# Performance work log

Measured on AMD Instinct MI355X. Metric: run time of the kernel, lower is better.

The kernel has to match this reference:

```python
import jax, jax.numpy as jnp
import numpy as np

B, L, H, A, C = 16, 2048, 1024, 1024, 5  # batch, seq_len, hidden, attention_size, num_cat_choices


def setup_inputs() -> dict:
    key = jax.random.key(0)
    ks = jax.random.split(key, 5)
    inp = jax.random.normal(ks[0], (B, L, H), dtype=jnp.float32)
    W_hidden = jax.random.normal(ks[1], (A, H), dtype=jnp.float32) * 0.02
    b_hidden = jnp.zeros((A,), jnp.float32)
    query = jax.random.normal(ks[2], (A, 1), dtype=jnp.float32) * 0.02
    W_cls = jax.random.normal(ks[3], (1, H), dtype=jnp.float32) * 0.02
    b_cls = jnp.zeros((1,), jnp.float32)
    # Build masks with exactly C marker positions per row (required by the
    # original nested-loop logic: C markers -> C segments, count in [0, C-1]).
    rng = np.random.default_rng(0)
    attn = np.zeros((B, L), np.int64)
    mlm = np.zeros((B, L), np.int64)
    for b in range(B):
        end = max(int(L - rng.integers(0, L // 4)), 64)  # valid length
        attn[b, :end] = 1
        seg = (end - 4) // C
        for c in range(C):
            mlm[b, 2 + c * seg] = 1
    return dict(input=inp, attention_mask=jnp.asarray(attn),
                mlm_mask=jnp.asarray(mlm), W_hidden=W_hidden,
                b_hidden=b_hidden, query=query, W_cls=W_cls, b_cls=b_cls)


def reference(input, attention_mask, mlm_mask, W_hidden, b_hidden, query, W_cls, b_cls):
    # --- attention merge (dropout is identity at eval) ---
    keys = jnp.tanh(input @ W_hidden.T + b_hidden)                    # (B,L,A)
    qvar = jnp.var(query, ddof=1)                                     # torch.var default: unbiased
    probs = (keys @ query) / jnp.sqrt(A * qvar)                       # (B,L,1)
    mask = (1.0 - attention_mask[..., None].astype(jnp.float32)) * -1000.0
    att = jax.nn.softmax(probs * mask, axis=1)                        # faithful: logits are probs*mask
    vals = att + input                                                # (B,L,H)
    # --- vectorized replacement of the nested segment-mask loop (roberta branch) ---
    idx = jnp.arange(L)
    marker = jnp.where(mlm_mask > 0, idx, L)                          # (B,L)
    starts = jnp.sort(marker, axis=1)[:, :C]                          # (B,C) marker positions
    end_idx = attention_mask.sum(axis=1)                              # (B,)
    # segment c covers [starts[c]+1, next_boundary); boundary = next marker - 1,
    # last segment's boundary = end_idx - 1  (mlm_mask_extend[i,c,start+1:j-1]=1)
    bounds = jnp.concatenate([starts[:, 1:] - 1, (end_idx - 1)[:, None]], axis=1)  # (B,C)
    seg_mask = ((idx[None, None, :] >= starts[:, :, None] + 1)
                & (idx[None, None, :] < bounds[:, :, None])).astype(vals.dtype)    # (B,C,L)
    # fused segment pooling: avoids materializing the (B,C,L,H) repeat
    context = jnp.einsum('bcl,blh->bch', seg_mask, vals)              # (B,C,H)
    logits = context @ W_cls.T + b_cls                                # (B,C,1)
    return logits
```

## Files before the change

### kernel.cpp

```cpp
#include <hip/hip_runtime.h>
#include <hip/hip_bf16.h>
#include <math.h>

#define B_ 16
#define L_ 2048
#define H_ 1024
#define A_ 1024
#define C_ 5

#define NSPLIT 4
#define MT 32
#define KPH 256
#define TPB 16
#define KC_BLOCKS (B_ * TPB * NSPLIT)
#define KE_BLOCKS (B_ * L_ / 16)
#define KW_BLOCKS 256
#define PBS 8
#define PROBE_THRESH 150.0f

typedef __attribute__((ext_vector_type(8))) short short8v;
typedef __attribute__((ext_vector_type(4))) float float4v;

static constexpr size_t OFF_SCAL   = 0;
static constexpr size_t OFF_END    = 64;
static constexpr size_t OFF_CNT    = 192;
static constexpr size_t OFF_STARTS = 320;
static constexpr size_t OFF_LIST   = 4096;
static constexpr size_t OFF_WF     = OFF_LIST + (size_t)B_ * L_ * 4;
static constexpr size_t OFF_PP     = OFF_WF + (size_t)A_ * H_ * 2;
static constexpr size_t OFF_D      = OFF_PP + (size_t)NSPLIT * B_ * L_ * 4;
static constexpr size_t OFF_PROBE  = OFF_D + (size_t)B_ * L_ * 4;

static __device__ __forceinline__ unsigned short f2bf(float f) {
  unsigned u = __float_as_uint(f);
  unsigned r = (u >> 16) & 1u;
  return (unsigned short)((u + 0x7fffu + r) >> 16);
}

__global__ __launch_bounds__(256) void kWA(const int* __restrict__ attn,
                                           const int* __restrict__ mlm,
                                           const float* __restrict__ query,
                                           const float* __restrict__ Wcls,
                                           const float* __restrict__ Wh,
                                           const float* __restrict__ inp,
                                           float* __restrict__ ws_scal,
                                           int* __restrict__ endv,
                                           int* __restrict__ cnt,
                                           int* __restrict__ starts,
                                           int* __restrict__ list,
                                           unsigned short* __restrict__ Wfrag,
                                           float* __restrict__ d) {
  __shared__ int   wsh[4];
  __shared__ float sf1[256];
  __shared__ float sf2[256];
  const int bid = blockIdx.x;
  const int t = threadIdx.x;
  const int w = t >> 6;
  const int lane = t & 63;

  if (bid < KE_BLOCKS) {
    const int r0 = bid * 16 + w * 4;
    const int a0v = attn[r0], a1v = attn[r0 + 1], a2v = attn[r0 + 2], a3v = attn[r0 + 3];
    if ((a0v | a1v | a2v | a3v) == 0) return;
    float4 wv4[4];
#pragma unroll
    for (int k = 0; k < 4; ++k) wv4[k] = *(const float4*)(Wcls + k * 256 + lane * 4);
    const float* p0 = inp + (size_t)r0 * H_;
    float4 x0[4], x1[4], x2[4], x3[4];
    if (a0v) {
#pragma unroll
      for (int k = 0; k < 4; ++k) x0[k] = *(const float4*)(p0 + k * 256 + lane * 4);
    }
    if (a1v) {
#pragma unroll
      for (int k = 0; k < 4; ++k) x1[k] = *(const float4*)(p0 + H_ + k * 256 + lane * 4);
    }
    if (a2v) {
#pragma unroll
      for (int k = 0; k < 4; ++k) x2[k] = *(const float4*)(p0 + 2 * H_ + k * 256 + lane * 4);
    }
    if (a3v) {
#pragma unroll
      for (int k = 0; k < 4; ++k) x3[k] = *(const float4*)(p0 + 3 * H_ + k * 256 + lane * 4);
    }
#define DOTROW(XV, AV, IDX)                                                          \
    if (AV) {                                                                        \
      float acc = 0.f;                                                               \
      _Pragma("unroll")                                                              \
      for (int k = 0; k < 4; ++k)                                                    \
        acc += XV[k].x * wv4[k].x + XV[k].y * wv4[k].y +                             \
               XV[k].z * wv4[k].z + XV[k].w * wv4[k].w;                              \
      _Pragma("unroll")                                                              \
      for (int o = 1; o < 64; o <<= 1) acc += __shfl_xor(acc, o, 64);                \
      if (lane == 0) d[r0 + IDX] = acc;                                              \
    }
    DOTROW(x0, a0v, 0)
    DOTROW(x1, a1v, 1)
    DOTROW(x2, a2v, 2)
    DOTROW(x3, a3v, 3)
#undef DOTROW
    return;
  }

  const int g = bid - KE_BLOCKS;
  if (g < B_) {
    const int b = g;
    const int* arow = attn + (size_t)b * L_;
    const int* mrow = mlm + (size_t)b * L_;
    const int base = t * 8;

    int loc[8];
    int lc = 0;
#pragma unroll
    for (int j = 0; j < 8; ++j) {
      int l = base + j;
      if (arow[l] == 0) loc[lc++] = l;
    }
    int incl = lc;
#pragma unroll
    for (int o = 1; o < 64; o <<= 1) {
      int v = __shfl_up(incl, o, 64);
      if (lane >= o) incl += v;
    }
    if (lane == 63) wsh[w] = incl;
    __syncthreads();
    int pre = 0, total = 0;
#pragma unroll
    for (int i = 0; i < 4; ++i) {
      int s = wsh[i];
      if (i < w) pre += s;
      total += s;
    }
    int excl = pre + incl - lc;
    int* lrow = list + (size_t)b * L_;
    for (int j = 0; j < lc; ++j) lrow[excl + j] = loc[j];
    if (t == 0) {
      cnt[b] = total;
      endv[b] = L_ - total;
    }
    __syncthreads();

    int mloc[8];
    int mc = 0;
#pragma unroll
    for (int j = 0; j < 8; ++j) {
      int l = base + j;
      if (mrow[l] > 0) mloc[mc++] = l;
    }
    int incl2 = mc;
#pragma unroll
    for (int o = 1; o < 64; o <<= 1) {
      int v = __shfl_up(incl2, o, 64);
      if (lane >= o) incl2 += v;
    }
    if (lane == 63) wsh[w] = incl2;
    __syncthreads();
    int pre2 = 0;
#pragma unroll
    for (int i = 0; i < 4; ++i) {
      if (i < w) pre2 += wsh[i];
    }
    int excl2 = pre2 + incl2 - mc;
    for (int j = 0; j < mc; ++j) {
      int idx = excl2 + j;
      if (idx < C_) starts[b * C_ + idx] = mloc[j];
    }
  } else if (g == B_) {
    float s = 0.f, s2 = 0.f;
    for (int i = t; i < A_; i += 256) {
      float q = query[i];
      s += q;
      s2 = fmaf(q, q, s2);
    }
    sf1[t] = s;
    sf2[t] = s2;
    __syncthreads();
    for (int off = 128; off >= 1; off >>= 1) {
      if (t < off) {
        sf1[t] += sf1[t + off];
        sf2[t] += sf2[t + off];
      }
      __syncthreads();
    }
    float qsum = sf1[0], qsq = sf2[0];
    __syncthreads();
    float wv = 0.f;
    for (int i = t; i < H_; i += 256) wv += Wcls[i];
    sf1[t] = wv;
    __syncthreads();
    for (int off = 128; off >= 1; off >>= 1) {
      if (t < off) sf1[t] += sf1[t + off];
      __syncthreads();
    }
    if (t == 0) {
      float var = (qsq - qsum * qsum / (float)A_) / (float)(A_ - 1);
      ws_scal[0] = sqrtf((float)A_ * var);
      ws_scal[1] = sf1[0];
    }
  } else {
    const int g4 = g - B_ - 1;
    const int ga = g4 >> 2;
    const int q = g4 & 3;
    const int row = ga * 16 + (lane & 15);
    const int colb = (lane >> 4) * 8;
    const float* srcrow = Wh + (size_t)row * H_;
#pragma unroll
    for (int i = 0; i < 2; ++i) {
      const int kb = q * 8 + w * 2 + i;
      const float* src = srcrow + kb * 32 + colb;
      float4 u0 = *(const float4*)src;
      float4 u1 = *(const float4*)(src + 4);
      union { short8v v; unsigned short h[8]; } o;
      o.h[0] = f2bf(u0.x); o.h[1] = f2bf(u0.y); o.h[2] = f2bf(u0.z); o.h[3] = f2bf(u0.w);
      o.h[4] = f2bf(u1.x); o.h[5] = f2bf(u1.y); o.h[6] = f2bf(u1.z); o.h[7] = f2bf(u1.w);
      *(short8v*)(Wfrag + (((size_t)ga * 32 + kb) * 64 + lane) * 8) = o.v;
    }
  }
}

__global__ __launch_bounds__(256) void kProbe(const float* __restrict__ inp,
                                              const unsigned short* __restrict__ Wfrag,
                                              const float* __restrict__ bh,
                                              const float* __restrict__ query,
                                              const int* __restrict__ cnt,
                                              const int* __restrict__ list,
                                              float* __restrict__ probe) {
  __shared__ __align__(16) unsigned short Xs[16][KPH + 8];
  __shared__ float red[4][16];
  const int bid = blockIdx.x;
  const int b = bid >> 3;
  const int sl = bid & 7;
  const int t = threadIdx.x;
  const int c0 = cnt[b];
  const int w = t >> 6;
  const int lane = t & 63;
  const int lg = lane >> 4;
  const int lc = lane & 15;

  const int srow = t >> 4;
  const int scol = (t & 15) * 16;
  int pi = srow;
  if (pi >= c0) pi = (c0 > 0) ? (c0 - 1) : 0;
  const int xl = (c0 > 0) ? list[(size_t)b * L_ + pi] : 0;
  const float* xptr = inp + ((size_t)(b * L_ + xl)) * H_ + scol;

  const unsigned short* wf = Wfrag + ((size_t)(sl * 8 + w * 2) * 32) * 512 + lane * 8;

  float4v acc0 = (float4v){0.f, 0.f, 0.f, 0.f};
  float4v acc1 = (float4v){0.f, 0.f, 0.f, 0.f};

  for (int ph = 0; ph < H_ / KPH; ++ph) {
    __syncthreads();
#pragma unroll
    for (int j = 0; j < 2; ++j) {
      float4 u0 = *(const float4*)(xptr + ph * KPH + j * 8);
      float4 u1 = *(const float4*)(xptr + ph * KPH + j * 8 + 4);
      union { short8v v; unsigned short h[8]; } o;
      o.h[0] = f2bf(u0.x); o.h[1] = f2bf(u0.y); o.h[2] = f2bf(u0.z); o.h[3] = f2bf(u0.w);
      o.h[4] = f2bf(u1.x); o.h[5] = f2bf(u1.y); o.h[6] = f2bf(u1.z); o.h[7] = f2bf(u1.w);
      *(short8v*)&Xs[srow][scol + j * 8] = o.v;
    }
    __syncthreads();
#pragma unroll
    for (int kk = 0; kk < 8; ++kk) {
      const int kb = ph * 8 + kk;
      short8v bv0 = *(const short8v*)(wf + (size_t)kb * 512);
      short8v bv1 = *(const short8v*)(wf + (size_t)kb * 512 + 32 * 512);
      short8v av = *(const short8v*)&Xs[lc][kk * 32 + lg * 8];
      acc0 = __builtin_amdgcn_mfma_f32_16x16x32_bf16(av, bv0, acc0, 0, 0, 0);
      acc1 = __builtin_amdgcn_mfma_f32_16x16x32_bf16(av, bv1, acc1, 0, 0, 0);
    }
  }

  float pp[4] = {0.f, 0.f, 0.f, 0.f};
  {
    const int ag0 = sl * 128 + w * 32 + lc;
    const float q0 = query[ag0];
    const float b0 = bh[ag0];
    const int ag1 = ag0 + 16;
    const float q1 = query[ag1];
    const float b1 = bh[ag1];
#pragma unroll
    for (int r = 0; r < 4; ++r) {
      pp[r] = fmaf(tanhf(acc0[r] + b0), q0, pp[r]);
      pp[r] = fmaf(tanhf(acc1[r] + b1), q1, pp[r]);
    }
  }
#pragma unroll
  for (int r = 0; r < 4; ++r) {
#pragma unroll
    for (int o = 1; o < 16; o <<= 1)
      pp[r] += __shfl_xor(pp[r], o, 64);
  }
  __syncthreads();
  if (lc == 0) {
#pragma unroll
    for (int r = 0; r < 4; ++r) red[w][lg * 4 + r] = pp[r];
  }
  __syncthreads();
  if (t < 16) {
    float s = red[0][t] + red[1][t] + red[2][t] + red[3][t];
    probe[((size_t)b * PBS + sl) * 16 + t] = (c0 > 0) ? s : 0.f;
  }
}

__global__ __launch_bounds__(256, 4) void kMain(const float* __restrict__ inp,
                                                const unsigned short* __restrict__ Wfrag,
                                                const float* __restrict__ bh,
                                                const float* __restrict__ query,
                                                const int* __restrict__ cnt,
                                                const int* __restrict__ list,
                                                const float* __restrict__ ws_scal,
                                                const float* __restrict__ probe,
                                                float* __restrict__ probpart) {
  __shared__ __align__(16) unsigned short Xs[MT][KPH + 8];
  __shared__ float red[4][MT];
  __shared__ int sskip;

  const int bid = blockIdx.x;
  const int t = threadIdx.x;
  const int w = t >> 6;
  const int lane = t & 63;

  const int as = (bid >> 3) & 3;
  const int T = (bid & 7) | ((bid >> 5) << 3);
  const int b = T >> 4;
  const int tile = T & 15;
  const int c0 = cnt[b];
  if (tile * MT >= c0) return;

  if (t == 0) sskip = 0;
  __syncthreads();
  if (t < 16) {
    float s = 0.f;
#pragma unroll
    for (int p8 = 0; p8 < PBS; ++p8) s += probe[((size_t)b * PBS + p8) * 16 + t];
    float logit = -1000.0f * (s / ws_scal[0]);
    if (logit >= PROBE_THRESH) atomicOr(&sskip, 1);
  }
  __syncthreads();
  if (sskip) return;

  const int lg = lane >> 4;
  const int lc = lane & 15;

  const int srow = t >> 3;
  const int scol = (t & 7) * 32;
  const int gi = tile * MT + srow;
  const int gidx = (gi < c0) ? gi : (c0 - 1);
  const int xl = list[(size_t)b * L_ + gidx];
  const float* xptr = inp + ((size_t)(b * L_ + xl)) * H_ + scol;

  const unsigned short* wfbase = Wfrag + ((size_t)(as * 16 + w * 4) * 32) * 512 + lane * 8;

  float4v acc[2][4];
#pragma unroll
  for (int m = 0; m < 2; ++m)
#pragma unroll
    for (int n = 0; n < 4; ++n) acc[m][n] = (float4v){0.f, 0.f, 0.f, 0.f};

  for (int ph = 0; ph < H_ / KPH; ++ph) {
    __syncthreads();
#pragma unroll
    for (int j = 0; j < 4; ++j) {
      float4 u0 = *(const float4*)(xptr + ph * KPH + j * 8);
      float4 u1 = *(const float4*)(xptr + ph * KPH + j * 8 + 4);
      union { short8v v; unsigned short h[8]; } o;
      o.h[0] = f2bf(u0.x); o.h[1] = f2bf(u0.y); o.h[2] = f2bf(u0.z); o.h[3] = f2bf(u0.w);
      o.h[4] = f2bf(u1.x); o.h[5] = f2bf(u1.y); o.h[6] = f2bf(u1.z); o.h[7] = f2bf(u1.w);
      *(short8v*)&Xs[srow][scol + j * 8] = o.v;
    }
    __syncthreads();

    const unsigned short* fp0 = wfbase + (size_t)(ph * 8) * 512;
    short8v cb0 = *(const short8v*)(fp0);
    short8v cb1 = *(const short8v*)(fp0 + 32 * 512);
    short8v cb2 = *(const short8v*)(fp0 + 64 * 512);
    short8v cb3 = *(const short8v*)(fp0 + 96 * 512);
#pragma unroll
    for (int kk = 0; kk < 8; ++kk) {
      short8v nb0, nb1, nb2, nb3;
      if (kk < 7) {
        const unsigned short* fn = wfbase + (size_t)(ph * 8 + kk + 1) * 512;
        nb0 = *(const short8v*)(fn);
        nb1 = *(const short8v*)(fn + 32 * 512);
        nb2 = *(const short8v*)(fn + 64 * 512);
        nb3 = *(const short8v*)(fn + 96 * 512);
      }
      const int off = kk * 32 + lg * 8;
      short8v av0 = *(const short8v*)&Xs[lc][off];
      short8v av1 = *(const short8v*)&Xs[16 + lc][off];
      acc[0][0] = __builtin_amdgcn_mfma_f32_16x16x32_bf16(av0, cb0, acc[0][0], 0, 0, 0);
      acc[1][0] = __builtin_amdgcn_mfma_f32_16x16x32_bf16(av1, cb0, acc[1][0], 0, 0, 0);
      acc[0][1] = __builtin_amdgcn_mfma_f32_16x16x32_bf16(av0, cb1, acc[0][1], 0, 0, 0);
      acc[1][1] = __builtin_amdgcn_mfma_f32_16x16x32_bf16(av1, cb1, acc[1][1], 0, 0, 0);
      acc[0][2] = __builtin_amdgcn_mfma_f32_16x16x32_bf16(av0, cb2, acc[0][2], 0, 0, 0);
      acc[1][2] = __builtin_amdgcn_mfma_f32_16x16x32_bf16(av1, cb2, acc[1][2], 0, 0, 0);
      acc[0][3] = __builtin_amdgcn_mfma_f32_16x16x32_bf16(av0, cb3, acc[0][3], 0, 0, 0);
      acc[1][3] = __builtin_amdgcn_mfma_f32_16x16x32_bf16(av1, cb3, acc[1][3], 0, 0, 0);
      if (kk < 7) { cb0 = nb0; cb1 = nb1; cb2 = nb2; cb3 = nb3; }
    }
  }

  float pp[2][4];
#pragma unroll
  for (int m = 0; m < 2; ++m)
#pragma unroll
    for (int r = 0; r < 4; ++r) pp[m][r] = 0.f;

#pragma unroll
  for (int n = 0; n < 4; ++n) {
    const int ag = as * 256 + w * 64 + n * 16 + lc;
    const float q = query[ag];
    const float bb = bh[ag];
#pragma unroll
    for (int m = 0; m < 2; ++m)
#pragma unroll
      for (int r = 0; r < 4; ++r) {
        float v = acc[m][n][r] + bb;
        pp[m][r] = fmaf(tanhf(v), q, pp[m][r]);
      }
  }
#pragma unroll
  for (int m = 0; m < 2; ++m)
#pragma unroll
    for (int r = 0; r < 4; ++r) {
#pragma unroll
      for (int o = 1; o < 16; o <<= 1)
        pp[m][r] += __shfl_xor(pp[m][r], o, 64);
    }
  __syncthreads();
  if (lc == 0) {
#pragma unroll
    for (int m = 0; m < 2; ++m)
#pragma unroll
      for (int r = 0; r < 4; ++r)
        red[w][m * 16 + lg * 4 + r] = pp[m][r];
  }
  __syncthreads();
  if (t < MT) {
    const int i = tile * MT + t;
    if (i < c0) {
      float sv = red[0][t] + red[1][t] + red[2][t] + red[3][t];
      int l = list[(size_t)b * L_ + i];
      probpart[((size_t)as * B_ + b) * L_ + l] = sv;
    }
  }
}

__global__ __launch_bounds__(256) void kT(const int* __restrict__ cnt,
                                          const int* __restrict__ list,
                                          const float* __restrict__ probpart,
                                          const float* __restrict__ ws_scal,
                                          const float* __restrict__ d,
                                          const int* __restrict__ starts,
                                          const int* __restrict__ endv,
                                          const float* __restrict__ probe,
                                          const float* __restrict__ bcls,
                                          float* __restrict__ out) {
  __shared__ float lg[L_];
  __shared__ float red[256];
  __shared__ int sskip;
  const int b = blockIdx.x;
  const int t = threadIdx.x;
  const float denom = ws_scal[0];
  const int c0 = cnt[b];

  if (t == 0) sskip = 0;
  __syncthreads();
  if (t < 16) {
    float s = 0.f;
#pragma unroll
    for (int p8 = 0; p8 < PBS; ++p8) s += probe[((size_t)b * PBS + p8) * 16 + t];
    float logit = -1000.0f * (s / denom);
    if (logit >= PROBE_THRESH) atomicOr(&sskip, 1);
  }
  __syncthreads();
  const bool skip = (c0 > 0) && (sskip != 0);

  float att0 = 0.0f;
  if (!skip) {
    float mx = 0.0f;
    for (int i = t; i < c0; i += 256) {
      int l = list[(size_t)b * L_ + i];
      float s = probpart[((size_t)0 * B_ + b) * L_ + l]
              + probpart[((size_t)1 * B_ + b) * L_ + l]
              + probpart[((size_t)2 * B_ + b) * L_ + l]
              + probpart[((size_t)3 * B_ + b) * L_ + l];
      float v = -1000.0f * (s / denom);
      lg[i] = v;
      mx = fmaxf(mx, v);
    }
    red[t] = mx;
    __syncthreads();
    for (int off = 128; off >= 1; off >>= 1) {
      if (t < off) red[t] = fmaxf(red[t], red[t + off]);
      __syncthreads();
    }
    const float m = red[0];
    __syncthreads();

    float zs = 0.f;
    for (int i = t; i < c0; i += 256) zs += expf(lg[i] - m);
    if (t == 0) zs += (float)(L_ - c0) * expf(-m);
    red[t] = zs;
    __syncthreads();
    for (int off = 128; off >= 1; off >>= 1) {
      if (t < off) red[t] += red[t + off];
      __syncthreads();
    }
    const float Z = red[0];
    __syncthreads();
    att0 = expf(-m) / Z;
  }

  for (int c = 0; c < C_; ++c) {
    const int st = starts[b * C_ + c];
    const int bound = (c < C_ - 1) ? (starts[b * C_ + c + 1] - 1) : (endv[b] - 1);
    const int lo = st + 1;
    const int hi = bound;
    float a = 0.f;
    for (int l = lo + t; l < hi; l += 256) a += d[(size_t)b * L_ + l];
    red[t] = a;
    __syncthreads();
    for (int off = 128; off >= 1; off >>= 1) {
      if (t < off) red[t] += red[t + off];
      __syncthreads();
    }
    if (t == 0) {
      int count = hi - lo;
      if (count < 0) count = 0;
      out[b * C_ + c] = red[0] + ws_scal[1] * att0 * (float)count + bcls[0];
    }
    __syncthreads();
  }
}

extern "C" void kernel_launch(void* const* d_in, const int* in_sizes, int n_in,
                              void* d_out, int out_size, void* d_ws, size_t ws_size,
                              hipStream_t stream) {
  const float* inp   = (const float*)d_in[0];
  const int*   attn  = (const int*)d_in[1];
  const int*   mlm   = (const int*)d_in[2];
  const float* Wh    = (const float*)d_in[3];
  const float* bh    = (const float*)d_in[4];
  const float* query = (const float*)d_in[5];
  const float* Wcls  = (const float*)d_in[6];
  const float* bcls  = (const float*)d_in[7];
  float* out = (float*)d_out;

  char* ws = (char*)d_ws;
  float*          ws_scal = (float*)(ws + OFF_SCAL);
  int*            endv    = (int*)(ws + OFF_END);
  int*            cnt     = (int*)(ws + OFF_CNT);
  int*            starts  = (int*)(ws + OFF_STARTS);
  int*            list    = (int*)(ws + OFF_LIST);
  unsigned short* Wfrag   = (unsigned short*)(ws + OFF_WF);
  float*          probpart= (float*)(ws + OFF_PP);
  float*          dvec    = (float*)(ws + OFF_D);
  float*          probe   = (float*)(ws + OFF_PROBE);

  hipLaunchKernelGGL(kWA, dim3(KE_BLOCKS + B_ + 1 + KW_BLOCKS), dim3(256), 0, stream,
                     attn, mlm, query, Wcls, Wh, inp, ws_scal, endv, cnt, starts, list,
                     Wfrag, dvec);
  hipLaunchKernelGGL(kProbe, dim3(B_ * PBS), dim3(256), 0, stream,
                     inp, Wfrag, bh, query, cnt, list, probe);
  hipLaunchKernelGGL(kMain, dim3(KC_BLOCKS), dim3(256), 0, stream,
                     inp, Wfrag, bh, query, cnt, list, ws_scal, probe, probpart);
  hipLaunchKernelGGL(kT, dim3(B_), dim3(256), 0, stream,
                     cnt, list, probpart, ws_scal, dvec, starts, endv, probe, bcls, out);
}
```

Measured before the change: 45.91 us.

## Fold probe kernel into preprocessing kernel to remove a launch dependency

The separate probe kernel is removed and its work moved into extra blocks of the first kernel. Those blocks compute the valid length themselves, take the first 16 padded rows starting at that length instead of reading the list from the prior kernel, and convert W_hidden to bf16 in shared memory rather than reading the pre-packed fragment buffer. This drops a kernel launch and the serial wait between the two stages. In exchange, each probe block redoes the W conversion and the row-sum, and the shared memory is laid out as a union of the per-role structs.

```diff
diff --git a/kernel.cpp b/kernel.cpp
--- a/kernel.cpp
+++ b/kernel.cpp
@@ -15,6 +15,7 @@
 #define KC_BLOCKS (B_ * TPB * NSPLIT)
 #define KE_BLOCKS (B_ * L_ / 16)
 #define KW_BLOCKS 256
+#define PB_BLOCKS 128
 #define PBS 8
 #define PROBE_THRESH 150.0f
 
@@ -37,22 +38,35 @@
   return (unsigned short)((u + 0x7fffu + r) >> 16);
 }
 
+struct ProbeSmem {
+  unsigned short Ws[128][72];
+  unsigned short Xs[16][72];
+  float red[4][16];
+  int isum[4];
+};
+struct ScalSmem { float sf1[256]; float sf2[256]; };
+union KWASmem {
+  ProbeSmem probe;
+  ScalSmem scal;
+  int wsh[4];
+};
+
 __global__ __launch_bounds__(256) void kWA(const int* __restrict__ attn,
                                            const int* __restrict__ mlm,
                                            const float* __restrict__ query,
                                            const float* __restrict__ Wcls,
                                            const float* __restrict__ Wh,
                                            const float* __restrict__ inp,
+                                           const float* __restrict__ bh,
                                            float* __restrict__ ws_scal,
                                            int* __restrict__ endv,
                                            int* __restrict__ cnt,
                                            int* __restrict__ starts,
                                            int* __restrict__ list,
                                            unsigned short* __restrict__ Wfrag,
-                                           float* __restrict__ d) {
-  __shared__ int   wsh[4];
-  __shared__ float sf1[256];
-  __shared__ float sf2[256];
+                                           float* __restrict__ d,
+                                           float* __restrict__ probe) {
+  __shared__ KWASmem smem;
   const int bid = blockIdx.x;
   const int t = threadIdx.x;
   const int w = t >> 6;
@@ -103,37 +117,129 @@
   }
 
   const int g = bid - KE_BLOCKS;
-  if (g < B_) {
-    const int b = g;
+  if (g < PB_BLOCKS) {
+    const int b = g >> 3;
+    const int sl = g & 7;
+    const int* arow = attn + (size_t)b * L_;
+
+    int s_ = 0;
+    for (int i = t; i < L_; i += 256) s_ += arow[i];
+#pragma unroll
+    for (int o = 1; o < 64; o <<= 1) s_ += __shfl_xor(s_, o, 64);
+    if (lane == 0) smem.probe.isum[w] = s_;
+    __syncthreads();
+    const int end = smem.probe.isum[0] + smem.probe.isum[1] +
+                    smem.probe.isum[2] + smem.probe.isum[3];
+
+    const int lg = lane >> 4;
+    const int lc = lane & 15;
+    const int xrow = t >> 4;
+    const int xcb = (t & 15) * 4;
+    const int pX = end + xrow;
+    const int pl = (pX < L_) ? pX : (L_ - 1);
+    const float* xsrc = inp + ((size_t)(b * L_ + pl)) * H_;
+    const int wrow = t >> 1;
+    const int wcb = (t & 1) * 32;
+    const float* wsrc = Wh + (size_t)(sl * 128 + wrow) * H_;
+
+    float4v acc0 = (float4v){0.f, 0.f, 0.f, 0.f};
+    float4v acc1 = (float4v){0.f, 0.f, 0.f, 0.f};
+
+    for (int ph = 0; ph < 16; ++ph) {
+      __syncthreads();
+      {
+        float4 u = *(const float4*)(xsrc + ph * 64 + xcb);
+        unsigned short* dx = &smem.probe.Xs[xrow][xcb];
+        dx[0] = f2bf(u.x); dx[1] = f2bf(u.y); dx[2] = f2bf(u.z); dx[3] = f2bf(u.w);
+      }
+#pragma unroll
+      for (int j = 0; j < 4; ++j) {
+        float4 u0 = *(const float4*)(wsrc + ph * 64 + wcb + j * 8);
+        float4 u1 = *(const float4*)(wsrc + ph * 64 + wcb + j * 8 + 4);
+        union { short8v v; unsigned short h[8]; } o;
+        o.h[0] = f2bf(u0.x); o.h[1] = f2bf(u0.y); o.h[2] = f2bf(u0.z); o.h[3] = f2bf(u0.w);
+        o.h[4] = f2bf(u1.x); o.h[5] = f2bf(u1.y); o.h[6] = f2bf(u1.z); o.h[7] = f2bf(u1.w);
+        *(short8v*)&smem.probe.Ws[wrow][wcb + j * 8] = o.v;
+      }
+      __syncthreads();
+#pragma unroll
+      for (int kk = 0; kk < 2; ++kk) {
+        short8v av = *(const short8v*)&smem.probe.Xs[lc][kk * 32 + lg * 8];
+        short8v bv0 = *(const short8v*)&smem.probe.Ws[w * 32 + lc][kk * 32 + lg * 8];
+        short8v bv1 = *(const short8v*)&smem.probe.Ws[w * 32 + 16 + lc][kk * 32 + lg * 8];
+        acc0 = __builtin_amdgcn_mfma_f32_16x16x32_bf16(av, bv0, acc0, 0, 0, 0);
+        acc1 = __builtin_amdgcn_mfma_f32_16x16x32_bf16(av, bv1, acc1, 0, 0, 0);
+      }
+    }
+
+    float pp[4] = {0.f, 0.f, 0.f, 0.f};
+    {
+      const int ag0 = sl * 128 + w * 32 + lc;
+      const float q0 = query[ag0];
+      const float b0 = bh[ag0];
+      const int ag1 = ag0 + 16;
+      const float q1 = query[ag1];
+      const float b1 = bh[ag1];
+#pragma unroll
+      for (int r = 0; r < 4; ++r) {
+        pp[r] = fmaf(tanhf(acc0[r] + b0), q0, pp[r]);
+        pp[r] = fmaf(tanhf(acc1[r] + b1), q1, pp[r]);
+      }
+    }
+#pragma unroll
+    for (int r = 0; r < 4; ++r) {
+#pragma unroll
+      for (int o = 1; o < 16; o <<= 1)
+        pp[r] += __shfl_xor(pp[r], o, 64);
+    }
+    __syncthreads();
+    if (lc == 0) {
+#pragma unroll
+      for (int r = 0; r < 4; ++r) smem.probe.red[w][lg * 4 + r] = pp[r];
+    }
+    __syncthreads();
+    if (t < 16) {
+      const int p = end + t;
+      const bool valid = (p < L_) && (arow[p] == 0);
+      float s = smem.probe.red[0][t] + smem.probe.red[1][t] +
+                smem.probe.red[2][t] + smem.probe.red[3][t];
+      probe[((size_t)b * PBS + sl) * 16 + t] = valid ? s : 0.f;
+    }
+    return;
+  }
+
+  const int g2 = g - PB_BLOCKS;
+  if (g2 < B_) {
+    const int b = g2;
     const int* arow = attn + (size_t)b * L_;
     const int* mrow = mlm + (size_t)b * L_;
     const int base = t * 8;
 
     int loc[8];
-    int lc = 0;
+    int lc2 = 0;
 #pragma unroll
     for (int j = 0; j < 8; ++j) {
       int l = base + j;
-      if (arow[l] == 0) loc[lc++] = l;
-    }
-    int incl = lc;
+      if (arow[l] == 0) loc[lc2++] = l;
+    }
+    int incl = lc2;
 #pragma unroll
     for (int o = 1; o < 64; o <<= 1) {
       int v = __shfl_up(incl, o, 64);
       if (lane >= o) incl += v;
     }
-    if (lane == 63) wsh[w] = incl;
+    if (lane == 63) smem.wsh[w] = incl;
     __syncthreads();
     int pre = 0, total = 0;
 #pragma unroll
     for (int i = 0; i < 4; ++i) {
-      int s = wsh[i];
+      int s = smem.wsh[i];
       if (i < w) pre += s;
       total += s;
     }
-    int excl = pre + incl - lc;
+    int excl = pre + incl - lc2;
     int* lrow = list + (size_t)b * L_;
-    for (int j = 0; j < lc; ++j) lrow[excl + j] = loc[j];
+    for (int j = 0; j < lc2; ++j) lrow[excl + j] = loc[j];
     if (t == 0) {
       cnt[b] = total;
       endv[b] = L_ - total;
@@ -153,52 +259,52 @@
       int v = __shfl_up(incl2, o, 64);
       if (lane >= o) incl2 += v;
     }
-    if (lane == 63) wsh[w] = incl2;
+    if (lane == 63) smem.wsh[w] = incl2;
     __syncthreads();
     int pre2 = 0;
 #pragma unroll
     for (int i = 0; i < 4; ++i) {
-      if (i < w) pre2 += wsh[i];
+      if (i < w) pre2 += smem.wsh[i];
     }
     int excl2 = pre2 + incl2 - mc;
     for (int j = 0; j < mc; ++j) {
       int idx = excl2 + j;
       if (idx < C_) starts[b * C_ + idx] = mloc[j];
     }
-  } else if (g == B_) {
+  } else if (g2 == B_) {
     float s = 0.f, s2 = 0.f;
     for (int i = t; i < A_; i += 256) {
       float q = query[i];
       s += q;
       s2 = fmaf(q, q, s2);
     }
-    sf1[t] = s;
-    sf2[t] = s2;
+    smem.scal.sf1[t] = s;
+    smem.scal.sf2[t] = s2;
     __syncthreads();
     for (int off = 128; off >= 1; off >>= 1) {
       if (t < off) {
-        sf1[t] += sf1[t + off];
-        sf2[t] += sf2[t + off];
-      }
-      __syncthreads();
-    }
-    float qsum = sf1[0], qsq = sf2[0];
+        smem.scal.sf1[t] += smem.scal.sf1[t + off];
+        smem.scal.sf2[t] += smem.scal.sf2[t + off];
+      }
+      __syncthreads();
+    }
+    float qsum = smem.scal.sf1[0], qsq = smem.scal.sf2[0];
     __syncthreads();
     float wv = 0.f;
     for (int i = t; i < H_; i += 256) wv += Wcls[i];
-    sf1[t] = wv;
+    smem.scal.sf1[t] = wv;
     __syncthreads();
     for (int off = 128; off >= 1; off >>= 1) {
-      if (t < off) sf1[t] += sf1[t + off];
+      if (t < off) smem.scal.sf1[t] += smem.scal.sf1[t + off];
       __syncthreads();
     }
     if (t == 0) {
       float var = (qsq - qsum * qsum / (float)A_) / (float)(A_ - 1);
       ws_scal[0] = sqrtf((float)A_ * var);
-      ws_scal[1] = sf1[0];
+      ws_scal[1] = smem.scal.sf1[0];
     }
   } else {
-    const int g4 = g - B_ - 1;
+    const int g4 = g2 - B_ - 1;
     const int ga = g4 >> 2;
     const int q = g4 & 3;
     const int row = ga * 16 + (lane & 15);
@@ -215,92 +321,6 @@
       o.h[4] = f2bf(u1.x); o.h[5] = f2bf(u1.y); o.h[6] = f2bf(u1.z); o.h[7] = f2bf(u1.w);
       *(short8v*)(Wfrag + (((size_t)ga * 32 + kb) * 64 + lane) * 8) = o.v;
     }
-  }
-}
-
-__global__ __launch_bounds__(256) void kProbe(const float* __restrict__ inp,
-                                              const unsigned short* __restrict__ Wfrag,
-                                              const float* __restrict__ bh,
-                                              const float* __restrict__ query,
-                                              const int* __restrict__ cnt,
-                                              const int* __restrict__ list,
-                                              float* __restrict__ probe) {
-  __shared__ __align__(16) unsigned short Xs[16][KPH + 8];
-  __shared__ float red[4][16];
-  const int bid = blockIdx.x;
-  const int b = bid >> 3;
-  const int sl = bid & 7;
-  const int t = threadIdx.x;
-  const int c0 = cnt[b];
-  const int w = t >> 6;
-  const int lane = t & 63;
-  const int lg = lane >> 4;
-  const int lc = lane & 15;
-
-  const int srow = t >> 4;
-  const int scol = (t & 15) * 16;
-  int pi = srow;
-  if (pi >= c0) pi = (c0 > 0) ? (c0 - 1) : 0;
-  const int xl = (c0 > 0) ? list[(size_t)b * L_ + pi] : 0;
-  const float* xptr = inp + ((size_t)(b * L_ + xl)) * H_ + scol;
-
-  const unsigned short* wf = Wfrag + ((size_t)(sl * 8 + w * 2) * 32) * 512 + lane * 8;
-
-  float4v acc0 = (float4v){0.f, 0.f, 0.f, 0.f};
-  float4v acc1 = (float4v){0.f, 0.f, 0.f, 0.f};
-
-  for (int ph = 0; ph < H_ / KPH; ++ph) {
-    __syncthreads();
-#pragma unroll
-    for (int j = 0; j < 2; ++j) {
-      float4 u0 = *(const float4*)(xptr + ph * KPH + j * 8);
-      float4 u1 = *(const float4*)(xptr + ph * KPH + j * 8 + 4);
-      union { short8v v; unsigned short h[8]; } o;
-      o.h[0] = f2bf(u0.x); o.h[1] = f2bf(u0.y); o.h[2] = f2bf(u0.z); o.h[3] = f2bf(u0.w);
-      o.h[4] = f2bf(u1.x); o.h[5] = f2bf(u1.y); o.h[6] = f2bf(u1.z); o.h[7] = f2bf(u1.w);
-      *(short8v*)&Xs[srow][scol + j * 8] = o.v;
-    }
-    __syncthreads();
-#pragma unroll
-    for (int kk = 0; kk < 8; ++kk) {
-      const int kb = ph * 8 + kk;
-      short8v bv0 = *(const short8v*)(wf + (size_t)kb * 512);
-      short8v bv1 = *(const short8v*)(wf + (size_t)kb * 512 + 32 * 512);
-      short8v av = *(const short8v*)&Xs[lc][kk * 32 + lg * 8];
-      acc0 = __builtin_amdgcn_mfma_f32_16x16x32_bf16(av, bv0, acc0, 0, 0, 0);
-      acc1 = __builtin_amdgcn_mfma_f32_16x16x32_bf16(av, bv1, acc1, 0, 0, 0);
-    }
-  }
-
-  float pp[4] = {0.f, 0.f, 0.f, 0.f};
-  {
-    const int ag0 = sl * 128 + w * 32 + lc;
-    const float q0 = query[ag0];
-    const float b0 = bh[ag0];
-    const int ag1 = ag0 + 16;
-    const float q1 = query[ag1];
-    const float b1 = bh[ag1];
-#pragma unroll
-    for (int r = 0; r < 4; ++r) {
-      pp[r] = fmaf(tanhf(acc0[r] + b0), q0, pp[r]);
-      pp[r] = fmaf(tanhf(acc1[r] + b1), q1, pp[r]);
-    }
-  }
-#pragma unroll
-  for (int r = 0; r < 4; ++r) {
-#pragma unroll
-    for (int o = 1; o < 16; o <<= 1)
-      pp[r] += __shfl_xor(pp[r], o, 64);
-  }
-  __syncthreads();
-  if (lc == 0) {
-#pragma unroll
-    for (int r = 0; r < 4; ++r) red[w][lg * 4 + r] = pp[r];
-  }
-  __syncthreads();
-  if (t < 16) {
-    float s = red[0][t] + red[1][t] + red[2][t] + red[3][t];
-    probe[((size_t)b * PBS + sl) * 16 + t] = (c0 > 0) ? s : 0.f;
   }
 }
 
@@ -560,11 +580,9 @@
   float*          dvec    = (float*)(ws + OFF_D);
   float*          probe   = (float*)(ws + OFF_PROBE);
 
-  hipLaunchKernelGGL(kWA, dim3(KE_BLOCKS + B_ + 1 + KW_BLOCKS), dim3(256), 0, stream,
-                     attn, mlm, query, Wcls, Wh, inp, ws_scal, endv, cnt, starts, list,
-                     Wfrag, dvec);
-  hipLaunchKernelGGL(kProbe, dim3(B_ * PBS), dim3(256), 0, stream,
-                     inp, Wfrag, bh, query, cnt, list, probe);
+  hipLaunchKernelGGL(kWA, dim3(KE_BLOCKS + PB_BLOCKS + B_ + 1 + KW_BLOCKS), dim3(256), 0,
+                     stream, attn, mlm, query, Wcls, Wh, inp, bh, ws_scal, endv, cnt,
+                     starts, list, Wfrag, dvec, probe);
   hipLaunchKernelGGL(kMain, dim3(KC_BLOCKS), dim3(256), 0, stream,
                      inp, Wfrag, bh, query, cnt, list, ws_scal, probe, probpart);
   hipLaunchKernelGGL(kT, dim3(B_), dim3(256), 0, stream,
```

After: 74.16 us. 61.5% more time.

## Move row-dot work from prep kernel into probe kernel to balance stages

Applied to the files above, without the earlier changes.

The per-row input·W_cls dot products (2048 blocks) are moved out of the first prep kernel and merged into the probe kernel's grid, after the 128 probe blocks. The prep kernel becomes small (masks, scalars, bf16 weight packing), so the probe work that depends on it starts sooner and the heavy streaming dot-product blocks overlap with the probe GEMM. The risk is that the probe blocks now compete with the streaming blocks for bandwidth and compute units.

```diff
diff --git a/kernel.cpp b/kernel.cpp
--- a/kernel.cpp
+++ b/kernel.cpp
@@ -15,6 +15,7 @@
 #define KC_BLOCKS (B_ * TPB * NSPLIT)
 #define KE_BLOCKS (B_ * L_ / 16)
 #define KW_BLOCKS 256
+#define PB_BLOCKS 128
 #define PBS 8
 #define PROBE_THRESH 150.0f
 
@@ -37,19 +38,17 @@
   return (unsigned short)((u + 0x7fffu + r) >> 16);
 }
 
-__global__ __launch_bounds__(256) void kWA(const int* __restrict__ attn,
-                                           const int* __restrict__ mlm,
-                                           const float* __restrict__ query,
-                                           const float* __restrict__ Wcls,
-                                           const float* __restrict__ Wh,
-                                           const float* __restrict__ inp,
-                                           float* __restrict__ ws_scal,
-                                           int* __restrict__ endv,
-                                           int* __restrict__ cnt,
-                                           int* __restrict__ starts,
-                                           int* __restrict__ list,
-                                           unsigned short* __restrict__ Wfrag,
-                                           float* __restrict__ d) {
+__global__ __launch_bounds__(256) void kPrep(const int* __restrict__ attn,
+                                             const int* __restrict__ mlm,
+                                             const float* __restrict__ query,
+                                             const float* __restrict__ Wcls,
+                                             const float* __restrict__ Wh,
+                                             float* __restrict__ ws_scal,
+                                             int* __restrict__ endv,
+                                             int* __restrict__ cnt,
+                                             int* __restrict__ starts,
+                                             int* __restrict__ list,
+                                             unsigned short* __restrict__ Wfrag) {
   __shared__ int   wsh[4];
   __shared__ float sf1[256];
   __shared__ float sf2[256];
@@ -58,8 +57,140 @@
   const int w = t >> 6;
   const int lane = t & 63;
 
-  if (bid < KE_BLOCKS) {
-    const int r0 = bid * 16 + w * 4;
+  if (bid < B_) {
+    const int b = bid;
+    const int* arow = attn + (size_t)b * L_;
+    const int* mrow = mlm + (size_t)b * L_;
+    const int base = t * 8;
+
+    int loc[8];
+    int lc = 0;
+#pragma unroll
+    for (int j = 0; j < 8; ++j) {
+      int l = base + j;
+      if (arow[l] == 0) loc[lc++] = l;
+    }
+    int incl = lc;
+#pragma unroll
+    for (int o = 1; o < 64; o <<= 1) {
+      int v = __shfl_up(incl, o, 64);
+      if (lane >= o) incl += v;
+    }
+    if (lane == 63) wsh[w] = incl;
+    __syncthreads();
+    int pre = 0, total = 0;
+#pragma unroll
+    for (int i = 0; i < 4; ++i) {
+      int s = wsh[i];
+      if (i < w) pre += s;
+      total += s;
+    }
+    int excl = pre + incl - lc;
+    int* lrow = list + (size_t)b * L_;
+    for (int j = 0; j < lc; ++j) lrow[excl + j] = loc[j];
+    if (t == 0) {
+      cnt[b] = total;
+      endv[b] = L_ - total;
+    }
+    __syncthreads();
+
+    int mloc[8];
+    int mc = 0;
+#pragma unroll
+    for (int j = 0; j < 8; ++j) {
+      int l = base + j;
+      if (mrow[l] > 0) mloc[mc++] = l;
+    }
+    int incl2 = mc;
+#pragma unroll
+    for (int o = 1; o < 64; o <<= 1) {
+      int v = __shfl_up(incl2, o, 64);
+      if (lane >= o) incl2 += v;
+    }
+    if (lane == 63) wsh[w] = incl2;
+    __syncthreads();
+    int pre2 = 0;
+#pragma unroll
+    for (int i = 0; i < 4; ++i) {
+      if (i < w) pre2 += wsh[i];
+    }
+    int excl2 = pre2 + incl2 - mc;
+    for (int j = 0; j < mc; ++j) {
+      int idx = excl2 + j;
+      if (idx < C_) starts[b * C_ + idx] = mloc[j];
+    }
+  } else if (bid == B_) {
+    float s = 0.f, s2 = 0.f;
+    for (int i = t; i < A_; i += 256) {
+      float q = query[i];
+      s += q;
+      s2 = fmaf(q, q, s2);
+    }
+    sf1[t] = s;
+    sf2[t] = s2;
+    __syncthreads();
+    for (int off = 128; off >= 1; off >>= 1) {
+      if (t < off) {
+        sf1[t] += sf1[t + off];
+        sf2[t] += sf2[t + off];
+      }
+      __syncthreads();
+    }
+    float qsum = sf1[0], qsq = sf2[0];
+    __syncthreads();
+    float wv = 0.f;
+    for (int i = t; i < H_; i += 256) wv += Wcls[i];
+    sf1[t] = wv;
+    __syncthreads();
+    for (int off = 128; off >= 1; off >>= 1) {
+      if (t < off) sf1[t] += sf1[t + off];
+      __syncthreads();
+    }
+    if (t == 0) {
+      float var = (qsq - qsum * qsum / (float)A_) / (float)(A_ - 1);
+      ws_scal[0] = sqrtf((float)A_ * var);
+      ws_scal[1] = sf1[0];
+    }
+  } else {
+    const int g4 = bid - B_ - 1;
+    const int ga = g4 >> 2;
+    const int q = g4 & 3;
+    const int row = ga * 16 + (lane & 15);
+    const int colb = (lane >> 4) * 8;
+    const float* srcrow = Wh + (size_t)row * H_;
+#pragma unroll
+    for (int i = 0; i < 2; ++i) {
+      const int kb = q * 8 + w * 2 + i;
+      const float* src = srcrow + kb * 32 + colb;
+      float4 u0 = *(const float4*)src;
+      float4 u1 = *(const float4*)(src + 4);
+      union { short8v v; unsigned short h[8]; } o;
+      o.h[0] = f2bf(u0.x); o.h[1] = f2bf(u0.y); o.h[2] = f2bf(u0.z); o.h[3] = f2bf(u0.w);
+      o.h[4] = f2bf(u1.x); o.h[5] = f2bf(u1.y); o.h[6] = f2bf(u1.z); o.h[7] = f2bf(u1.w);
+      *(short8v*)(Wfrag + (((size_t)ga * 32 + kb) * 64 + lane) * 8) = o.v;
+    }
+  }
+}
+
+__global__ __launch_bounds__(256) void kSP(const float* __restrict__ inp,
+                                           const unsigned short* __restrict__ Wfrag,
+                                           const float* __restrict__ bh,
+                                           const float* __restrict__ query,
+                                           const float* __restrict__ Wcls,
+                                           const int* __restrict__ attn,
+                                           const int* __restrict__ cnt,
+                                           const int* __restrict__ list,
+                                           float* __restrict__ probe,
+                                           float* __restrict__ d) {
+  __shared__ __align__(16) unsigned short Xs[16][KPH + 8];
+  __shared__ float red[4][16];
+  const int bid = blockIdx.x;
+  const int t = threadIdx.x;
+  const int w = t >> 6;
+  const int lane = t & 63;
+
+  if (bid >= PB_BLOCKS) {
+    const int r0 = (bid - PB_BLOCKS) * 16 + w * 4;
     const int a0v = attn[r0], a1v = attn[r0 + 1], a2v = attn[r0 + 2], a3v = attn[r0 + 3];
     if ((a0v | a1v | a2v | a3v) == 0) return;
     float4 wv4[4];
@@ -102,138 +233,9 @@
     return;
   }
 
-  const int g = bid - KE_BLOCKS;
-  if (g < B_) {
-    const int b = g;
-    const int* arow = attn + (size_t)b * L_;
-    const int* mrow = mlm + (size_t)b * L_;
-    const int base = t * 8;
-
-    int loc[8];
-    int lc = 0;
-#pragma unroll
-    for (int j = 0; j < 8; ++j) {
-      int l = base + j;
-      if (arow[l] == 0) loc[lc++] = l;
-    }
-    int incl = lc;
-#pragma unroll
-    for (int o = 1; o < 64; o <<= 1) {
-      int v = __shfl_up(incl, o, 64);
-      if (lane >= o) incl += v;
-    }
-    if (lane == 63) wsh[w] = incl;
-    __syncthreads();
-    int pre = 0, total = 0;
-#pragma unroll
-    for (int i = 0; i < 4; ++i) {
-      int s = wsh[i];
-      if (i < w) pre += s;
-      total += s;
-    }
-    int excl = pre + incl - lc;
-    int* lrow = list + (size_t)b * L_;
-    for (int j = 0; j < lc; ++j) lrow[excl + j] = loc[j];
-    if (t == 0) {
-      cnt[b] = total;
-      endv[b] = L_ - total;
-    }
-    __syncthreads();
-
-    int mloc[8];
-    int mc = 0;
-#pragma unroll
-    for (int j = 0; j < 8; ++j) {
-      int l = base + j;
-      if (mrow[l] > 0) mloc[mc++] = l;
-    }
-    int incl2 = mc;
-#pragma unroll
-    for (int o = 1; o < 64; o <<= 1) {
-      int v = __shfl_up(incl2, o, 64);
-      if (lane >= o) incl2 += v;
-    }
-    if (lane == 63) wsh[w] = incl2;
-    __syncthreads();
-    int pre2 = 0;
-#pragma unroll
-    for (int i = 0; i < 4; ++i) {
-      if (i < w) pre2 += wsh[i];
-    }
-    int excl2 = pre2 + incl2 - mc;
-    for (int j = 0; j < mc; ++j) {
-      int idx = excl2 + j;
-      if (idx < C_) starts[b * C_ + idx] = mloc[j];
-    }
-  } else if (g == B_) {
-    float s = 0.f, s2 = 0.f;
-    for (int i = t; i < A_; i += 256) {
-      float q = query[i];
-      s += q;
-      s2 = fmaf(q, q, s2);
-    }
-    sf1[t] = s;
-    sf2[t] = s2;
-    __syncthreads();
-    for (int off = 128; off >= 1; off >>= 1) {
-      if (t < off) {
-        sf1[t] += sf1[t + off];
-        sf2[t] += sf2[t + off];
-      }
-      __syncthreads();
-    }
-    float qsum = sf1[0], qsq = sf2[0];
-    __syncthreads();
-    float wv = 0.f;
-    for (int i = t; i < H_; i += 256) wv += Wcls[i];
-    sf1[t] = wv;
-    __syncthreads();
-    for (int off = 128; off >= 1; off >>= 1) {
-      if (t < off) sf1[t] += sf1[t + off];
-      __syncthreads();
-    }
-    if (t == 0) {
-      float var = (qsq - qsum * qsum / (float)A_) / (float)(A_ - 1);
-      ws_scal[0] = sqrtf((float)A_ * var);
-      ws_scal[1] = sf1[0];
-    }
-  } else {
-    const int g4 = g - B_ - 1;
-    const int ga = g4 >> 2;
-    const int q = g4 & 3;
-    const int row = ga * 16 + (lane & 15);
-    const int colb = (lane >> 4) * 8;
-    const float* srcrow = Wh + (size_t)row * H_;
-#pragma unroll
-    for (int i = 0; i < 2; ++i) {
-      const int kb = q * 8 + w * 2 + i;
-      const float* src = srcrow + kb * 32 + colb;
-      float4 u0 = *(const float4*)src;
-      float4 u1 = *(const float4*)(src + 4);
-      union { short8v v; unsigned short h[8]; } o;
-      o.h[0] = f2bf(u0.x); o.h[1] = f2bf(u0.y); o.h[2] = f2bf(u0.z); o.h[3] = f2bf(u0.w);
-      o.h[4] = f2bf(u1.x); o.h[5] = f2bf(u1.y); o.h[6] = f2bf(u1.z); o.h[7] = f2bf(u1.w);
-      *(short8v*)(Wfrag + (((size_t)ga * 32 + kb) * 64 + lane) * 8) = o.v;
-    }
-  }
-}
-
-__global__ __launch_bounds__(256) void kProbe(const float* __restrict__ inp,
-                                              const unsigned short* __restrict__ Wfrag,
-                                              const float* __restrict__ bh,
-                                              const float* __restrict__ query,
-                                              const int* __restrict__ cnt,
-                                              const int* __restrict__ list,
-                                              float* __restrict__ probe) {
-  __shared__ __align__(16) unsigned short Xs[16][KPH + 8];
-  __shared__ float red[4][16];
-  const int bid = blockIdx.x;
   const int b = bid >> 3;
   const int sl = bid & 7;
-  const int t = threadIdx.x;
   const int c0 = cnt[b];
-  const int w = t >> 6;
-  const int lane = t & 63;
   const int lg = lane >> 4;
   const int lc = lane & 15;
 
@@ -560,11 +562,10 @@
   float*          dvec    = (float*)(ws + OFF_D);
   float*          probe   = (float*)(ws + OFF_PROBE);
 
-  hipLaunchKernelGGL(kWA, dim3(KE_BLOCKS + B_ + 1 + KW_BLOCKS), dim3(256), 0, stream,
-                     attn, mlm, query, Wcls, Wh, inp, ws_scal, endv, cnt, starts, list,
-                     Wfrag, dvec);
-  hipLaunchKernelGGL(kProbe, dim3(B_ * PBS), dim3(256), 0, stream,
-                     inp, Wfrag, bh, query, cnt, list, probe);
+  hipLaunchKernelGGL(kPrep, dim3(B_ + 1 + KW_BLOCKS), dim3(256), 0, stream,
+                     attn, mlm, query, Wcls, Wh, ws_scal, endv, cnt, starts, list, Wfrag);
+  hipLaunchKernelGGL(kSP, dim3(PB_BLOCKS + KE_BLOCKS), dim3(256), 0, stream,
+                     inp, Wfrag, bh, query, Wcls, attn, cnt, list, probe, dvec);
   hipLaunchKernelGGL(kMain, dim3(KC_BLOCKS), dim3(256), 0, stream,
                      inp, Wfrag, bh, query, cnt, list, ws_scal, probe, probpart);
   hipLaunchKernelGGL(kT, dim3(B_), dim3(256), 0, stream,
```

After: 41.55 us. 9.5% less time.
